# Kernel optimization log

Measured on AMD Instinct MI355X. Metric: run time of the kernel, lower is better.

Reference implementation:

```python
import jax, jax.numpy as jnp
import numpy as np

L, D, H, DH, I, S, B, MAXP, NFEAT = 4, 512, 4, 128, 128, 256, 128, 256, 6


def layer_norm(x, g, b):
    mu = jnp.mean(x, -1, keepdims=True)
    var = jnp.mean((x - mu) ** 2, -1, keepdims=True)
    return (x - mu) * jax.lax.rsqrt(var + 1e-12) * g + b


def setup_inputs() -> dict:
    key = jax.random.key(0)
    ks = iter(jax.random.split(key, 16))
    p = lambda shape: jax.random.normal(next(ks), shape, jnp.float32) * 0.02
    return dict(
        input_ids=jax.random.randint(next(ks), (B, S, NFEAT), 0, 64, jnp.int32),
        attn_mask=jnp.ones((B, S), jnp.float32),
        in_W=p((NFEAT, D)), in_b=jnp.zeros((D,), jnp.float32),
        tok_emb=p((D,)),  # token_type_embeddings row 0 (all-zero token type ids)
        emb_ln_g=jnp.ones((D,), jnp.float32), emb_ln_b=jnp.zeros((D,), jnp.float32),
        dist_emb=p((2 * MAXP - 1, DH)),
        Wq=p((L, D, D)), bq=jnp.zeros((L, D), jnp.float32),
        Wk=p((L, D, D)), bk=jnp.zeros((L, D), jnp.float32),
        Wv=p((L, D, D)), bv=jnp.zeros((L, D), jnp.float32),
        Wo=p((L, D, D)), bo=jnp.zeros((L, D), jnp.float32),
        ln1_g=jnp.ones((L, D), jnp.float32), ln1_b=jnp.zeros((L, D), jnp.float32),
        Wi=p((L, D, I)), bi=jnp.zeros((L, I), jnp.float32),
        Wo2=p((L, I, D)), bo2=jnp.zeros((L, D), jnp.float32),
        ln2_g=jnp.ones((L, D), jnp.float32), ln2_b=jnp.zeros((L, D), jnp.float32),
    )


def reference(input_ids, attn_mask, in_W, in_b, tok_emb, emb_ln_g, emb_ln_b,
              dist_emb, Wq, bq, Wk, bk, Wv, bv, Wo, bo, ln1_g, ln1_b,
              Wi, bi, Wo2, bo2, ln2_g, ln2_b):
    # in_linear on raw float features, then BertEmbeddings (no absolute pos emb
    # since position_embedding_type='relative_key_query'), token_type 0 + LN.
    x = input_ids.astype(jnp.float32) @ in_W + in_b          # [B,S,D]
    x = layer_norm(x + tok_emb, emb_ln_g, emb_ln_b)
    # relative position embeddings: distance l-r, table index shifted by MAXP-1
    pos = jnp.arange(S)
    pe = dist_emb[pos[:, None] - pos[None, :] + MAXP - 1]    # [S,S,DH]
    bias = (1.0 - attn_mask)[:, None, None, :] * jnp.float32(-1e9)
    scale = jnp.float32(1.0 / np.sqrt(DH))
    for l in range(L):
        q = (x @ Wq[l] + bq[l]).reshape(B, S, H, DH).transpose(0, 2, 1, 3)
        k = (x @ Wk[l] + bk[l]).reshape(B, S, H, DH).transpose(0, 2, 1, 3)
        v = (x @ Wv[l] + bv[l]).reshape(B, S, H, DH).transpose(0, 2, 1, 3)
        scores = jnp.einsum('bhld,bhrd->bhlr', q, k)
        scores = scores + jnp.einsum('bhld,lrd->bhlr', q, pe)  # relative_key_query: query term
        scores = scores + jnp.einsum('bhrd,lrd->bhlr', k, pe)  # key term
        probs = jax.nn.softmax(scores * scale + bias, axis=-1)
        ctx = jnp.einsum('bhlr,bhrd->bhld', probs, v)
        ctx = ctx.transpose(0, 2, 1, 3).reshape(B, S, D)
        x = layer_norm(x + ctx @ Wo[l] + bo[l], ln1_g[l], ln1_b[l])
        h = jax.nn.gelu(x @ Wi[l] + bi[l], approximate=False)
        x = layer_norm(x + h @ Wo2[l] + bo2[l], ln2_g[l], ln2_b[l])
    return x  # last_hidden_state [B,S,D]
```

## Files before the change

### kernel.cpp

```cpp
#include <hip/hip_runtime.h>

typedef unsigned short u16;
typedef __bf16 bf16x8 __attribute__((ext_vector_type(8)));
typedef float f32x4 __attribute__((ext_vector_type(4)));

__device__ __forceinline__ float b2f(u16 u) { return __uint_as_float(((unsigned)u) << 16); }
__device__ __forceinline__ u16 f2b(float f) {
  unsigned i = __float_as_uint(f);
  return (u16)((i + 0x7FFFu + ((i >> 16) & 1u)) >> 16);
}
__device__ __forceinline__ float sane(float x, float lim) {
  float y = fminf(fmaxf(x, -lim), lim);
  return (y != y) ? 0.0f : y;
}
__device__ __forceinline__ float wred(float x) {
#pragma unroll
  for (int m = 1; m < 64; m <<= 1) x += __shfl_xor(x, m, 64);
  return x;
}

__device__ __forceinline__ void bar_lgkm() {
  asm volatile("s_waitcnt lgkmcnt(0)" ::: "memory");
  __builtin_amdgcn_s_barrier();
  asm volatile("" ::: "memory");
}

__global__ void detect_dtype(const unsigned* __restrict__ g_ones, int* __restrict__ flag) {
  *flag = (g_ones[0] == 0x3F800000u) ? 1 : 0;
}

#define NSEG 23
struct CvtArgs {
  const void* src[NSEG];
  int start[NSEG + 1];
};
__global__ __launch_bounds__(256) void cvt_all(CvtArgs a, u16* __restrict__ dst,
                                               const int* __restrict__ flag) {
  const int i = blockIdx.x * 256 + threadIdx.x;
  if (i >= a.start[NSEG]) return;
  int k = 0;
#pragma unroll
  for (int s = 1; s < NSEG; ++s) k += (i >= a.start[s]) ? 1 : 0;
  const int j = i - a.start[k];
  u16 v;
  if (*flag) v = f2b(((const float*)a.src[k])[j]);
  else       v = ((const u16*)a.src[k])[j];
  dst[i] = v;
}

__global__ __launch_bounds__(256) void transpose_bf16(const u16* __restrict__ src,
                                                      u16* __restrict__ dst, int R, int C) {
  __shared__ u16 tile[32][33];
  const long zo = (long)blockIdx.z * R * C;
  src += zo; dst += zo;
  const int tx = threadIdx.x & 31, ty = threadIdx.x >> 5;
  const int c0 = blockIdx.x * 32, r0 = blockIdx.y * 32;
#pragma unroll
  for (int i = 0; i < 32; i += 8) tile[ty + i][tx] = src[(r0 + ty + i) * C + c0 + tx];
  __syncthreads();
#pragma unroll
  for (int i = 0; i < 32; i += 8) dst[(c0 + ty + i) * R + r0 + tx] = tile[tx][ty + i];
}

__global__ __launch_bounds__(256) void embed_ln(const int* __restrict__ ids,
    const u16* __restrict__ inW, const u16* __restrict__ inB, const u16* __restrict__ tokE,
    const u16* __restrict__ g, const u16* __restrict__ bb, u16* __restrict__ xb) {
  const int wave = threadIdx.x >> 6, lane = threadIdx.x & 63;
  const int n = blockIdx.x * 4 + wave;
  float idv[6];
#pragma unroll
  for (int f = 0; f < 6; ++f) idv[f] = (float)ids[n * 6 + f];
  float v[8]; float s = 0.f;
#pragma unroll
  for (int j = 0; j < 8; ++j) {
    const int d = j * 64 + lane;
    float a = b2f(inB[d]) + b2f(tokE[d]);
#pragma unroll
    for (int f = 0; f < 6; ++f) a += idv[f] * b2f(inW[f * 512 + d]);
    v[j] = a; s += a;
  }
  s = wred(s);
  const float mu = s * (1.f / 512.f);
  float q = 0.f;
#pragma unroll
  for (int j = 0; j < 8; ++j) { float t = v[j] - mu; q += t * t; }
  q = wred(q);
  const float rstd = rsqrtf(q * (1.f / 512.f) + 1e-12f);
#pragma unroll
  for (int j = 0; j < 8; ++j) {
    const int d = j * 64 + lane;
    xb[n * 512 + d] = f2b(sane((v[j] - mu) * rstd * b2f(g[d]) + b2f(bb[d]), 6e4f));
  }
}

__global__ __launch_bounds__(256) void add_ln(const u16* __restrict__ xin,
    const u16* __restrict__ add, const u16* __restrict__ g, const u16* __restrict__ bb,
    void* __restrict__ outp, const int* __restrict__ flag, int isfinal) {
  const int wave = threadIdx.x >> 6, lane = threadIdx.x & 63;
  const int n = blockIdx.x * 4 + wave;
  const int base = n * 512 + lane * 8;
  uint4 xa = *(const uint4*)&xin[base];
  uint4 aa = *(const uint4*)&add[base];
  const unsigned* xw = (const unsigned*)&xa;
  const unsigned* aw = (const unsigned*)&aa;
  float v[8]; float s = 0.f;
#pragma unroll
  for (int w = 0; w < 4; ++w) {
    float x0 = b2f((u16)(xw[w] & 0xffff)) + b2f((u16)(aw[w] & 0xffff));
    float x1 = b2f((u16)(xw[w] >> 16)) + b2f((u16)(aw[w] >> 16));
    v[w * 2] = x0; v[w * 2 + 1] = x1; s += x0 + x1;
  }
  s = wred(s);
  const float mu = s * (1.f / 512.f);
  float qs = 0.f;
#pragma unroll
  for (int j = 0; j < 8; ++j) { float t = v[j] - mu; qs += t * t; }
  qs = wred(qs);
  const float rstd = rsqrtf(qs * (1.f / 512.f) + 1e-12f);
  uint4 ga = *(const uint4*)&g[lane * 8];
  uint4 ba = *(const uint4*)&bb[lane * 8];
  const unsigned* gw = (const unsigned*)&ga;
  const unsigned* bw = (const unsigned*)&ba;
  float y[8];
#pragma unroll
  for (int w = 0; w < 4; ++w) {
    y[w * 2]     = sane((v[w * 2] - mu) * rstd * b2f((u16)(gw[w] & 0xffff)) + b2f((u16)(bw[w] & 0xffff)), 6e4f);
    y[w * 2 + 1] = sane((v[w * 2 + 1] - mu) * rstd * b2f((u16)(gw[w] >> 16)) + b2f((u16)(bw[w] >> 16)), 6e4f);
  }
  if (isfinal && *flag) {
    float* of = (float*)outp;
    float4 o0, o1;
    o0.x = y[0]; o0.y = y[1]; o0.z = y[2]; o0.w = y[3];
    o1.x = y[4]; o1.y = y[5]; o1.z = y[6]; o1.w = y[7];
    *(float4*)&of[base] = o0;
    *(float4*)&of[base + 4] = o1;
  } else {
    uint4 o;
    unsigned* ow = (unsigned*)&o;
#pragma unroll
    for (int w = 0; w < 4; ++w)
      ow[w] = (unsigned)f2b(y[w * 2]) | ((unsigned)f2b(y[w * 2 + 1]) << 16);
    *(uint4*)&((u16*)outp)[base] = o;
  }
}

enum { EPI_ROW, EPI_GELU, EPI_QKH, EPI_VT, EPI_B2, EPI_B3 };

typedef __attribute__((address_space(1))) const char gld_g;
typedef __attribute__((address_space(3))) char gld_l;

template <int EPI>
__global__ __launch_bounds__(256)
void gemm_bt(const u16* __restrict__ A, const u16* __restrict__ BT,
             const u16* __restrict__ bias, u16* __restrict__ out, int K, int ldo) {
  __shared__ alignas(16) u16 sT[2 * 128 * 64];
  u16* sA = sT;
  u16* sB = sT + 128 * 64;
  const int tid = threadIdx.x;
  const int wave = tid >> 6, lane = tid & 63;
  const int quad = lane >> 4, li = lane & 15;
  const int m0 = blockIdx.x * 128, n0 = blockIdx.y * 128;
  const u16* Ab = A + (size_t)m0 * K;
  const u16* Bb = BT + (size_t)n0 * K;
  const int wm = wave >> 1, wn = wave & 1;
  const int lrow = lane >> 3;
  const int lchk = (lane & 7) ^ lrow;
  f32x4 acc[4][4] = {};
  for (int kt = 0; kt < K; kt += 64) {
    if (kt) __syncthreads();
#pragma unroll
    for (int i = 0; i < 4; ++i) {
      const int r = wave * 32 + i * 8 + lrow;
      __builtin_amdgcn_global_load_lds(
          (gld_g*)(Ab + (size_t)r * K + kt + lchk * 8),
          (gld_l*)&sA[(wave * 32 + i * 8) * 64], 16, 0, 0);
      __builtin_amdgcn_global_load_lds(
          (gld_g*)(Bb + (size_t)r * K + kt + lchk * 8),
          (gld_l*)&sB[(wave * 32 + i * 8) * 64], 16, 0, 0);
    }
    asm volatile("s_waitcnt vmcnt(0)" ::: "memory");
    __syncthreads();
#pragma unroll
    for (int h = 0; h < 2; ++h) {
      bf16x8 aF[4], bF[4];
#pragma unroll
      for (int mt = 0; mt < 4; ++mt) {
        const int r = wm * 64 + mt * 16 + li;
        aF[mt] = *(const bf16x8*)&sA[r * 64 + ((h * 32 + quad * 8) ^ ((r & 7) << 3))];
      }
#pragma unroll
      for (int nt = 0; nt < 4; ++nt) {
        const int r = wn * 64 + nt * 16 + li;
        bF[nt] = *(const bf16x8*)&sB[r * 64 + ((h * 32 + quad * 8) ^ ((r & 7) << 3))];
      }
#pragma unroll
      for (int mt = 0; mt < 4; ++mt)
#pragma unroll
        for (int nt = 0; nt < 4; ++nt)
          acc[mt][nt] = __builtin_amdgcn_mfma_f32_16x16x32_bf16(aF[mt], bF[nt], acc[mt][nt], 0, 0, 0);
    }
  }
  if constexpr (EPI == EPI_VT) {
    __syncthreads();
#pragma unroll
    for (int mt = 0; mt < 4; ++mt)
#pragma unroll
      for (int nt = 0; nt < 4; ++nt)
#pragma unroll
        for (int r = 0; r < 4; ++r) {
          const int ml = wm * 64 + mt * 16 + quad * 4 + r;
          const int nl = wn * 64 + nt * 16 + li;
          float v = sane(acc[mt][nt][r] + b2f(bias[n0 + nl]), 6e4f);
          sT[nl * 128 + (ml ^ ((nl & 7) << 3))] = f2b(v);
        }
    __syncthreads();
    const int bht = (m0 >> 8) * 4 + (n0 >> 7);
    const int s0 = m0 & 255;
    const int dh = tid >> 1, half = tid & 1;
    u16* orow = out + ((size_t)bht * 128 + dh) * 256 + s0 + half * 64;
#pragma unroll
    for (int i = 0; i < 8; ++i) {
      const int idx = dh * 128 + ((half * 64 + i * 8) ^ ((dh & 7) << 3));
      *(uint4*)&orow[i * 8] = *(const uint4*)&sT[idx];
    }
  } else if constexpr (EPI == EPI_B2 || EPI == EPI_B3) {
#pragma unroll
    for (int mt = 0; mt < 4; ++mt) {
#pragma unroll
      for (int nt = 0; nt < 4; ++nt) {
#pragma unroll
        for (int r = 0; r < 4; ++r) {
          const int m = m0 + wm * 64 + mt * 16 + quad * 4 + r;
          const int n = n0 + wn * 64 + nt * 16 + li;
          float v = sane(acc[mt][nt][r], 1e4f);
          const int ll = m & 255;
          if constexpr (EPI == EPI_B2) {
            const int rr2 = ll - n + 255;
            if ((unsigned)rr2 < 256u) out[(size_t)m * 256 + rr2] = f2b(v);
          } else {
            const int lo = n + ll - 255;
            if ((unsigned)lo < 256u) out[(size_t)m * 256 + lo] = f2b(v);
          }
        }
      }
    }
  } else {
#pragma unroll
    for (int mt = 0; mt < 4; ++mt) {
#pragma unroll
      for (int nt = 0; nt < 4; ++nt) {
#pragma unroll
        for (int r = 0; r < 4; ++r) {
          const int m = m0 + wm * 64 + mt * 16 + quad * 4 + r;
          const int n = n0 + wn * 64 + nt * 16 + li;
          float v = sane(acc[mt][nt][r] + b2f(bias[n]), 6e4f);
          if constexpr (EPI == EPI_GELU) v = 0.5f * v * (1.0f + erff(v * 0.70710678118654752f));
          if constexpr (EPI == EPI_ROW || EPI == EPI_GELU) {
            out[m * ldo + n] = f2b(v);
          } else {
            out[(((m >> 8) * 4 + (n >> 7)) * 256 + (m & 255)) * 128 + (n & 127)] = f2b(v);
          }
        }
      }
    }
  }
}

__global__ __launch_bounds__(256, 3)
void attn_kernel(const u16* __restrict__ qb, const u16* __restrict__ kb,
                 const u16* __restrict__ vtb, const u16* __restrict__ b2g,
                 const u16* __restrict__ b3g, const u16* __restrict__ mask,
                 u16* __restrict__ ctx) {
  __shared__ alignas(16) u16 sKV[9216];
  __shared__ alignas(16) u16 sP[16896];
  char* sPb = (char*)sP;
  const int tid = threadIdx.x;
  const int wave = tid >> 6, lane = tid & 63, quad = lane >> 4, li = lane & 15;
  const int lt = blockIdx.x;
  const int bh = blockIdx.y;
  const int b = bh >> 2, h = bh & 3;
  const int l0 = lt * 64;
  const u16* Qg = qb + (size_t)bh * 256 * 128;
  const u16* Kg = kb + (size_t)bh * 256 * 128;
  const u16* Vg = vtb + (size_t)bh * 128 * 256;
  const u16* B2g = b2g + (size_t)bh * 256 * 256;
  const u16* B3g = b3g + (size_t)bh * 256 * 256;
  const float scale = 0.08838834764831845f;

  const int krow = tid >> 2, kq4 = tid & 3;
  uint4 kreg[2][4];
#pragma unroll
  for (int i = 0; i < 4; ++i)
    kreg[0][i] = *(const uint4*)&Kg[krow * 128 + kq4 * 8 + i * 32];
  uint4 breg[2][2];
#pragma unroll
  for (int h2 = 0; h2 < 2; ++h2)
    breg[0][h2] = *(const uint4*)&B3g[(size_t)krow * 256 + l0 + kq4 * 16 + h2 * 8];

  bf16x8 aQ[4];
#pragma unroll
  for (int kt = 0; kt < 4; ++kt)
    aQ[kt] = *(const bf16x8*)&Qg[(l0 + wave * 16 + li) * 128 + kt * 32 + quad * 8];

  f32x4 sc[16] = {};
#pragma unroll
  for (int c = 0; c < 4; ++c) {
    if (c > 0) bar_lgkm();
#pragma unroll
    for (int i = 0; i < 4; ++i)
      *(uint4*)&sKV[krow * 136 + kq4 * 8 + i * 32] = kreg[c & 1][i];
#pragma unroll
    for (int h2 = 0; h2 < 2; ++h2)
      *(uint4*)&sPb[c * 8192 + ((krow * 128 + kq4 * 32 + h2 * 16) ^ ((krow & 7) << 4))] =
          breg[c & 1][h2];
    u16 b2v[16];
#pragma unroll
    for (int t2 = 0; t2 < 4; ++t2)
#pragma unroll
      for (int rr = 0; rr < 4; ++rr)
        b2v[t2 * 4 + rr] =
            B2g[(size_t)(l0 + wave * 16 + quad * 4 + rr) * 256 + c * 64 + t2 * 16 + li];
    if (c < 3) {
#pragma unroll
      for (int i = 0; i < 4; ++i)
        kreg[(c + 1) & 1][i] =
            *(const uint4*)&Kg[((c + 1) * 64 + krow) * 128 + kq4 * 8 + i * 32];
#pragma unroll
      for (int h2 = 0; h2 < 2; ++h2)
        breg[(c + 1) & 1][h2] =
            *(const uint4*)&B3g[(size_t)((c + 1) * 64 + krow) * 256 + l0 + kq4 * 16 + h2 * 8];
    }
    bar_lgkm();
    __builtin_amdgcn_s_setprio(1);
#pragma unroll
    for (int kt = 0; kt < 4; ++kt) {
#pragma unroll
      for (int nt = 0; nt < 4; ++nt) {
        bf16x8 bK = *(const bf16x8*)&sKV[(nt * 16 + li) * 136 + kt * 32 + quad * 8];
        sc[c * 4 + nt] = __builtin_amdgcn_mfma_f32_16x16x32_bf16(aQ[kt], bK, sc[c * 4 + nt], 0, 0, 0);
      }
    }
    __builtin_amdgcn_s_setprio(0);
#pragma unroll
    for (int t2 = 0; t2 < 4; ++t2)
#pragma unroll
      for (int rr = 0; rr < 4; ++rr) {
        const int myl = wave * 16 + quad * 4 + rr;
        const int R = t2 * 16 + li;
        float v3 = b2f(*(const u16*)&sPb[c * 8192 + ((R * 128 + myl * 2) ^ ((R & 7) << 4))]);
        float v2 = b2f(b2v[t2 * 4 + rr]);
        sc[c * 4 + t2][rr] += v2 + v3;
      }
  }

  const int vrow = tid >> 1, vhalf = tid & 1;
  uint4 vreg[2][4];
#pragma unroll
  for (int i = 0; i < 4; ++i)
    vreg[0][i] = *(const uint4*)&Vg[vrow * 256 + vhalf * 32 + i * 8];

  float mbv[16];
#pragma unroll
  for (int t = 0; t < 16; ++t)
    mbv[t] = (1.0f - b2f(mask[b * 256 + t * 16 + li])) * -1e9f;

#pragma unroll
  for (int t = 0; t < 16; ++t)
#pragma unroll
    for (int r = 0; r < 4; ++r) sc[t][r] = sane(sc[t][r] * scale + mbv[t], 2e9f);
#pragma unroll
  for (int r = 0; r < 4; ++r) {
    float mx = -3.0e38f;
#pragma unroll
    for (int t = 0; t < 16; ++t) mx = fmaxf(mx, sc[t][r]);
#pragma unroll
    for (int m = 1; m < 16; m <<= 1) mx = fmaxf(mx, __shfl_xor(mx, m, 64));
    float s = 0.f;
#pragma unroll
    for (int t = 0; t < 16; ++t) { float e = __expf(sc[t][r] - mx); sc[t][r] = e; s += e; }
#pragma unroll
    for (int m = 1; m < 16; m <<= 1) s += __shfl_xor(s, m, 64);
    const float inv = 1.f / s;
#pragma unroll
    for (int t = 0; t < 16; ++t) sc[t][r] *= inv;
  }

  bar_lgkm();
#pragma unroll
  for (int t = 0; t < 16; ++t)
#pragma unroll
    for (int r = 0; r < 4; ++r)
      sP[(wave * 16 + quad * 4 + r) * 264 + t * 16 + li] = f2b(sc[t][r]);

  f32x4 ct[8] = {};
#pragma unroll
  for (int c = 0; c < 4; ++c) {
    if (c > 0) bar_lgkm();
#pragma unroll
    for (int i = 0; i < 4; ++i)
      *(uint4*)&sKV[vrow * 72 + vhalf * 32 + i * 8] = vreg[c & 1][i];
    if (c < 3) {
#pragma unroll
      for (int i = 0; i < 4; ++i)
        vreg[(c + 1) & 1][i] =
            *(const uint4*)&Vg[vrow * 256 + (c + 1) * 64 + vhalf * 32 + i * 8];
    }
    bar_lgkm();
    __builtin_amdgcn_s_setprio(1);
#pragma unroll
    for (int ks = 0; ks < 2; ++ks) {
      bf16x8 aF = *(const bf16x8*)&sP[(wave * 16 + li) * 264 + c * 64 + ks * 32 + quad * 8];
#pragma unroll
      for (int nt = 0; nt < 8; ++nt) {
        bf16x8 bV = *(const bf16x8*)&sKV[(nt * 16 + li) * 72 + ks * 32 + quad * 8];
        ct[nt] = __builtin_amdgcn_mfma_f32_16x16x32_bf16(aF, bV, ct[nt], 0, 0, 0);
      }
    }
    __builtin_amdgcn_s_setprio(0);
  }

  bar_lgkm();
#pragma unroll
  for (int nt = 0; nt < 8; ++nt)
#pragma unroll
    for (int r = 0; r < 4; ++r)
      sP[(wave * 16 + quad * 4 + r) * 136 + nt * 16 + li] = f2b(sane(ct[nt][r], 1e4f));
  bar_lgkm();
  {
    const int row = tid >> 2, seg = tid & 3;
    u16* orow = ctx + ((size_t)(b * 256 + l0 + row)) * 512 + h * 128 + seg * 32;
    const u16* srow = &sP[row * 136 + seg * 32];
#pragma unroll
    for (int i = 0; i < 4; ++i)
      *(uint4*)&orow[i * 8] = *(const uint4*)&srow[i * 8];
  }
}

extern "C" void kernel_launch(void* const* d_in, const int* in_sizes, int n_in,
                              void* d_out, int out_size, void* d_ws, size_t ws_size,
                              hipStream_t stream) {
  (void)in_sizes; (void)n_in; (void)out_size; (void)ws_size;
  const int* ids = (const int*)d_in[0];

  static const int ns[NSEG] = {
      32768, 3072, 512, 512, 512, 512, 65408,
      1048576, 2048, 1048576, 2048, 1048576, 2048, 1048576, 2048,
      2048, 2048, 262144, 512, 262144, 2048, 2048, 2048
  };
  CvtArgs ca;
  int st[NSEG + 1];
  st[0] = 0;
  for (int k = 0; k < NSEG; ++k) { ca.src[k] = d_in[k + 1]; st[k + 1] = st[k] + ns[k]; }
  for (int k = 0; k <= NSEG; ++k) ca.start[k] = st[k];
  const int total = st[NSEG];

  char* W = (char*)d_ws;
  size_t off = 0;
  auto alloc = [&](size_t bytes) { void* p = W + off; off += (bytes + 255) & ~(size_t)255; return p; };
  u16* canon = (u16*)alloc((size_t)total * 2);
  int* flag  = (int*)alloc(256);
  const size_t ND = (size_t)32768 * 512;
  u16* xb   = (u16*)alloc(ND * 2);
  u16* qbf  = (u16*)alloc(ND * 2);
  u16* kbf  = (u16*)alloc(ND * 2);
  u16* vtb  = (u16*)alloc(ND * 2);
  u16* b2b  = (u16*)alloc((size_t)32768 * 256 * 2);
  u16* b3b  = (u16*)alloc((size_t)32768 * 256 * 2);
  u16* wqT  = (u16*)alloc((size_t)4 * 512 * 512 * 2);
  u16* wkT  = (u16*)alloc((size_t)4 * 512 * 512 * 2);
  u16* wvT  = (u16*)alloc((size_t)4 * 512 * 512 * 2);
  u16* woT  = (u16*)alloc((size_t)4 * 512 * 512 * 2);
  u16* wiT  = (u16*)alloc((size_t)4 * 512 * 128 * 2);
  u16* wo2T = (u16*)alloc((size_t)4 * 128 * 512 * 2);
  u16* ctxb = (u16*)d_out;

  const u16* mask = canon + st[0];
  const u16* inW  = canon + st[1];
  const u16* inB  = canon + st[2];
  const u16* tokE = canon + st[3];
  const u16* eg   = canon + st[4];
  const u16* ebb  = canon + st[5];
  const u16* de   = canon + st[6];
  const u16* Wq   = canon + st[7];
  const u16* bq   = canon + st[8];
  const u16* Wk   = canon + st[9];
  const u16* bk   = canon + st[10];
  const u16* Wv   = canon + st[11];
  const u16* bv   = canon + st[12];
  const u16* Wo   = canon + st[13];
  const u16* bo   = canon + st[14];
  const u16* l1g  = canon + st[15];
  const u16* l1b  = canon + st[16];
  const u16* Wi   = canon + st[17];
  const u16* bi   = canon + st[18];
  const u16* Wo2  = canon + st[19];
  const u16* bo2  = canon + st[20];
  const u16* l2g  = canon + st[21];
  const u16* l2b  = canon + st[22];

  dim3 B256(256);
  detect_dtype<<<1, 1, 0, stream>>>((const unsigned*)d_in[5], flag);
  cvt_all<<<(total + 255) / 256, B256, 0, stream>>>(ca, canon, flag);
  transpose_bf16<<<dim3(16, 16, 4), B256, 0, stream>>>(Wq, wqT, 512, 512);
  transpose_bf16<<<dim3(16, 16, 4), B256, 0, stream>>>(Wk, wkT, 512, 512);
  transpose_bf16<<<dim3(16, 16, 4), B256, 0, stream>>>(Wv, wvT, 512, 512);
  transpose_bf16<<<dim3(16, 16, 4), B256, 0, stream>>>(Wo, woT, 512, 512);
  transpose_bf16<<<dim3(4, 16, 4), B256, 0, stream>>>(Wi, wiT, 512, 128);
  transpose_bf16<<<dim3(16, 4, 4), B256, 0, stream>>>(Wo2, wo2T, 128, 512);
  embed_ln<<<8192, B256, 0, stream>>>(ids, inW, inB, tokE, eg, ebb, xb);

  for (int l = 0; l < 4; ++l) {
    gemm_bt<EPI_QKH><<<dim3(256, 4), B256, 0, stream>>>(xb, wqT + l * 512 * 512, bq + l * 512, qbf, 512, 0);
    gemm_bt<EPI_QKH><<<dim3(256, 4), B256, 0, stream>>>(xb, wkT + l * 512 * 512, bk + l * 512, kbf, 512, 0);
    gemm_bt<EPI_B2><<<dim3(256, 4), B256, 0, stream>>>(qbf, de, bq, b2b, 128, 0);
    gemm_bt<EPI_B3><<<dim3(256, 4), B256, 0, stream>>>(kbf, de, bk, b3b, 128, 0);
    gemm_bt<EPI_VT><<<dim3(256, 4), B256, 0, stream>>>(xb, wvT + l * 512 * 512, bv + l * 512, vtb, 512, 0);
    attn_kernel<<<dim3(4, 512), B256, 0, stream>>>(qbf, kbf, vtb, b2b, b3b, mask, ctxb);
    gemm_bt<EPI_ROW><<<dim3(256, 4), B256, 0, stream>>>(ctxb, woT + l * 512 * 512, bo + l * 512, qbf, 512, 512);
    add_ln<<<8192, B256, 0, stream>>>(xb, qbf, l1g + l * 512, l1b + l * 512, xb, flag, 0);
    gemm_bt<EPI_GELU><<<dim3(256, 1), B256, 0, stream>>>(xb, wiT + l * 512 * 128, bi + l * 128, kbf, 512, 128);
    gemm_bt<EPI_ROW><<<dim3(256, 4), B256, 0, stream>>>(kbf, wo2T + l * 128 * 512, bo2 + l * 512, vtb, 128, 512);
    add_ln<<<8192, B256, 0, stream>>>(xb, vtb, l2g + l * 512, l2b + l * 512,
                                      (l == 3) ? d_out : (void*)xb, flag, (l == 3) ? 1 : 0);
  }
}
```

Baseline: 1.320 ms.

## Fuse QKV projection, band-limit relative-position GEMMs, chunk attention by head quarter

Merges the Q, K and V projection GEMMs into a single launch over a concatenated transposed weight, with per-column-block epilogues. Replaces the two full relative-position GEMMs with one band kernel that only computes the three 128-wide distance tiles each row block actually needs, dropping a quarter of that work. Interleaves the band GEMM and attention over four quarters of the batch-heads so the bias intermediates being consumed are smaller and more likely to stay cached. This adds launches per layer and adds branching in the fused epilogue.

```diff
diff --git a/kernel.cpp b/kernel.cpp
--- a/kernel.cpp
+++ b/kernel.cpp
@@ -49,10 +49,11 @@
 }
 
 __global__ __launch_bounds__(256) void transpose_bf16(const u16* __restrict__ src,
-                                                      u16* __restrict__ dst, int R, int C) {
+                                                      u16* __restrict__ dst, int R, int C,
+                                                      long dstride) {
   __shared__ u16 tile[32][33];
-  const long zo = (long)blockIdx.z * R * C;
-  src += zo; dst += zo;
+  src += (long)blockIdx.z * R * C;
+  dst += (long)blockIdx.z * dstride;
   const int tx = threadIdx.x & 31, ty = threadIdx.x >> 5;
   const int c0 = blockIdx.x * 32, r0 = blockIdx.y * 32;
 #pragma unroll
@@ -144,10 +145,55 @@
   }
 }
 
-enum { EPI_ROW, EPI_GELU, EPI_QKH, EPI_VT, EPI_B2, EPI_B3 };
+enum { EPI_ROW, EPI_GELU };
 
 typedef __attribute__((address_space(1))) const char gld_g;
 typedef __attribute__((address_space(3))) char gld_l;
+
+#define GEMM_PROLOG                                             \
+  const int tid = threadIdx.x;                                  \
+  const int wave = tid >> 6, lane = tid & 63;                   \
+  const int quad = lane >> 4, li = lane & 15;                   \
+  const int wm = wave >> 1, wn = wave & 1;                      \
+  const int lrow = lane >> 3;                                   \
+  const int lchk = (lane & 7) ^ lrow;
+
+#define GEMM_KLOOP(KK)                                                              \
+  f32x4 acc[4][4] = {};                                                             \
+  for (int kt = 0; kt < (KK); kt += 64) {                                           \
+    if (kt) __syncthreads();                                                        \
+    _Pragma("unroll")                                                               \
+    for (int i = 0; i < 4; ++i) {                                                   \
+      const int r = wave * 32 + i * 8 + lrow;                                       \
+      __builtin_amdgcn_global_load_lds(                                             \
+          (gld_g*)(Ab + (size_t)r * (KK) + kt + lchk * 8),                          \
+          (gld_l*)&sA[(wave * 32 + i * 8) * 64], 16, 0, 0);                         \
+      __builtin_amdgcn_global_load_lds(                                             \
+          (gld_g*)(Bb + (size_t)r * (KK) + kt + lchk * 8),                          \
+          (gld_l*)&sB[(wave * 32 + i * 8) * 64], 16, 0, 0);                         \
+    }                                                                               \
+    asm volatile("s_waitcnt vmcnt(0)" ::: "memory");                                \
+    __syncthreads();                                                                \
+    _Pragma("unroll")                                                               \
+    for (int h = 0; h < 2; ++h) {                                                   \
+      bf16x8 aF[4], bF[4];                                                          \
+      _Pragma("unroll")                                                             \
+      for (int mt = 0; mt < 4; ++mt) {                                              \
+        const int r = wm * 64 + mt * 16 + li;                                       \
+        aF[mt] = *(const bf16x8*)&sA[r * 64 + ((h * 32 + quad * 8) ^ ((r & 7) << 3))]; \
+      }                                                                             \
+      _Pragma("unroll")                                                             \
+      for (int nt = 0; nt < 4; ++nt) {                                              \
+        const int r = wn * 64 + nt * 16 + li;                                       \
+        bF[nt] = *(const bf16x8*)&sB[r * 64 + ((h * 32 + quad * 8) ^ ((r & 7) << 3))]; \
+      }                                                                             \
+      _Pragma("unroll")                                                             \
+      for (int mt = 0; mt < 4; ++mt)                                                \
+        _Pragma("unroll")                                                           \
+        for (int nt = 0; nt < 4; ++nt)                                              \
+          acc[mt][nt] = __builtin_amdgcn_mfma_f32_16x16x32_bf16(aF[mt], bF[nt], acc[mt][nt], 0, 0, 0); \
+    }                                                                               \
+  }
 
 template <int EPI>
 __global__ __launch_bounds__(256)
@@ -156,51 +202,42 @@
   __shared__ alignas(16) u16 sT[2 * 128 * 64];
   u16* sA = sT;
   u16* sB = sT + 128 * 64;
-  const int tid = threadIdx.x;
-  const int wave = tid >> 6, lane = tid & 63;
-  const int quad = lane >> 4, li = lane & 15;
+  GEMM_PROLOG
   const int m0 = blockIdx.x * 128, n0 = blockIdx.y * 128;
   const u16* Ab = A + (size_t)m0 * K;
   const u16* Bb = BT + (size_t)n0 * K;
-  const int wm = wave >> 1, wn = wave & 1;
-  const int lrow = lane >> 3;
-  const int lchk = (lane & 7) ^ lrow;
-  f32x4 acc[4][4] = {};
-  for (int kt = 0; kt < K; kt += 64) {
-    if (kt) __syncthreads();
-#pragma unroll
-    for (int i = 0; i < 4; ++i) {
-      const int r = wave * 32 + i * 8 + lrow;
-      __builtin_amdgcn_global_load_lds(
-          (gld_g*)(Ab + (size_t)r * K + kt + lchk * 8),
-          (gld_l*)&sA[(wave * 32 + i * 8) * 64], 16, 0, 0);
-      __builtin_amdgcn_global_load_lds(
-          (gld_g*)(Bb + (size_t)r * K + kt + lchk * 8),
-          (gld_l*)&sB[(wave * 32 + i * 8) * 64], 16, 0, 0);
-    }
-    asm volatile("s_waitcnt vmcnt(0)" ::: "memory");
-    __syncthreads();
-#pragma unroll
-    for (int h = 0; h < 2; ++h) {
-      bf16x8 aF[4], bF[4];
-#pragma unroll
-      for (int mt = 0; mt < 4; ++mt) {
-        const int r = wm * 64 + mt * 16 + li;
-        aF[mt] = *(const bf16x8*)&sA[r * 64 + ((h * 32 + quad * 8) ^ ((r & 7) << 3))];
+  GEMM_KLOOP(K)
+#pragma unroll
+  for (int mt = 0; mt < 4; ++mt) {
+#pragma unroll
+    for (int nt = 0; nt < 4; ++nt) {
+#pragma unroll
+      for (int r = 0; r < 4; ++r) {
+        const int m = m0 + wm * 64 + mt * 16 + quad * 4 + r;
+        const int n = n0 + wn * 64 + nt * 16 + li;
+        float v = sane(acc[mt][nt][r] + b2f(bias[n]), 6e4f);
+        if constexpr (EPI == EPI_GELU) v = 0.5f * v * (1.0f + erff(v * 0.70710678118654752f));
+        out[m * ldo + n] = f2b(v);
       }
-#pragma unroll
-      for (int nt = 0; nt < 4; ++nt) {
-        const int r = wn * 64 + nt * 16 + li;
-        bF[nt] = *(const bf16x8*)&sB[r * 64 + ((h * 32 + quad * 8) ^ ((r & 7) << 3))];
-      }
-#pragma unroll
-      for (int mt = 0; mt < 4; ++mt)
-#pragma unroll
-        for (int nt = 0; nt < 4; ++nt)
-          acc[mt][nt] = __builtin_amdgcn_mfma_f32_16x16x32_bf16(aF[mt], bF[nt], acc[mt][nt], 0, 0, 0);
-    }
-  }
-  if constexpr (EPI == EPI_VT) {
+    }
+  }
+}
+
+__global__ __launch_bounds__(256)
+void gemm_qkv(const u16* __restrict__ A, const u16* __restrict__ BT,
+              const u16* __restrict__ bq, const u16* __restrict__ bk,
+              const u16* __restrict__ bv, u16* __restrict__ qo,
+              u16* __restrict__ ko, u16* __restrict__ vo) {
+  __shared__ alignas(16) u16 sT[2 * 128 * 64];
+  u16* sA = sT;
+  u16* sB = sT + 128 * 64;
+  GEMM_PROLOG
+  const int m0 = blockIdx.x * 128, n0 = blockIdx.y * 128;
+  const u16* Ab = A + (size_t)m0 * 512;
+  const u16* Bb = BT + (size_t)n0 * 512;
+  GEMM_KLOOP(512)
+  const int which = n0 >> 9, nb = n0 & 511;
+  if (which == 2) {
     __syncthreads();
 #pragma unroll
     for (int mt = 0; mt < 4; ++mt)
@@ -210,20 +247,22 @@
         for (int r = 0; r < 4; ++r) {
           const int ml = wm * 64 + mt * 16 + quad * 4 + r;
           const int nl = wn * 64 + nt * 16 + li;
-          float v = sane(acc[mt][nt][r] + b2f(bias[n0 + nl]), 6e4f);
+          float v = sane(acc[mt][nt][r] + b2f(bv[nb + nl]), 6e4f);
           sT[nl * 128 + (ml ^ ((nl & 7) << 3))] = f2b(v);
         }
     __syncthreads();
-    const int bht = (m0 >> 8) * 4 + (n0 >> 7);
+    const int bht = (m0 >> 8) * 4 + (nb >> 7);
     const int s0 = m0 & 255;
     const int dh = tid >> 1, half = tid & 1;
-    u16* orow = out + ((size_t)bht * 128 + dh) * 256 + s0 + half * 64;
+    u16* orow = vo + ((size_t)bht * 128 + dh) * 256 + s0 + half * 64;
 #pragma unroll
     for (int i = 0; i < 8; ++i) {
       const int idx = dh * 128 + ((half * 64 + i * 8) ^ ((dh & 7) << 3));
       *(uint4*)&orow[i * 8] = *(const uint4*)&sT[idx];
     }
-  } else if constexpr (EPI == EPI_B2 || EPI == EPI_B3) {
+  } else {
+    u16* o = which ? ko : qo;
+    const u16* bi = which ? bk : bq;
 #pragma unroll
     for (int mt = 0; mt < 4; ++mt) {
 #pragma unroll
@@ -231,35 +270,46 @@
 #pragma unroll
         for (int r = 0; r < 4; ++r) {
           const int m = m0 + wm * 64 + mt * 16 + quad * 4 + r;
-          const int n = n0 + wn * 64 + nt * 16 + li;
-          float v = sane(acc[mt][nt][r], 1e4f);
-          const int ll = m & 255;
-          if constexpr (EPI == EPI_B2) {
-            const int rr2 = ll - n + 255;
-            if ((unsigned)rr2 < 256u) out[(size_t)m * 256 + rr2] = f2b(v);
-          } else {
-            const int lo = n + ll - 255;
-            if ((unsigned)lo < 256u) out[(size_t)m * 256 + lo] = f2b(v);
-          }
+          const int n = nb + wn * 64 + nt * 16 + li;
+          float v = sane(acc[mt][nt][r] + b2f(bi[n]), 6e4f);
+          o[(((m >> 8) * 4 + (n >> 7)) * 256 + (m & 255)) * 128 + (n & 127)] = f2b(v);
         }
       }
     }
-  } else {
-#pragma unroll
-    for (int mt = 0; mt < 4; ++mt) {
-#pragma unroll
-      for (int nt = 0; nt < 4; ++nt) {
-#pragma unroll
-        for (int r = 0; r < 4; ++r) {
-          const int m = m0 + wm * 64 + mt * 16 + quad * 4 + r;
-          const int n = n0 + wn * 64 + nt * 16 + li;
-          float v = sane(acc[mt][nt][r] + b2f(bias[n]), 6e4f);
-          if constexpr (EPI == EPI_GELU) v = 0.5f * v * (1.0f + erff(v * 0.70710678118654752f));
-          if constexpr (EPI == EPI_ROW || EPI == EPI_GELU) {
-            out[m * ldo + n] = f2b(v);
-          } else {
-            out[(((m >> 8) * 4 + (n >> 7)) * 256 + (m & 255)) * 128 + (n & 127)] = f2b(v);
-          }
+  }
+}
+
+__global__ __launch_bounds__(256)
+void gemm_band(const u16* __restrict__ qq, const u16* __restrict__ kq,
+               const u16* __restrict__ de, u16* __restrict__ b2o,
+               u16* __restrict__ b3o) {
+  __shared__ alignas(16) u16 sT[2 * 128 * 64];
+  u16* sA = sT;
+  u16* sB = sT + 128 * 64;
+  GEMM_PROLOG
+  const int half = blockIdx.x >> 8;
+  const int mi = (blockIdx.x & 255) * 128;
+  const int s0 = mi & 255;
+  const int p0 = (half ? 128 - s0 : s0) + blockIdx.y * 128;
+  const u16* Ab = (half ? kq : qq) + (size_t)mi * 128;
+  const u16* Bb = de + (size_t)p0 * 128;
+  GEMM_KLOOP(128)
+#pragma unroll
+  for (int mt = 0; mt < 4; ++mt) {
+#pragma unroll
+    for (int nt = 0; nt < 4; ++nt) {
+#pragma unroll
+      for (int r = 0; r < 4; ++r) {
+        const int m = mi + wm * 64 + mt * 16 + quad * 4 + r;
+        const int n = p0 + wn * 64 + nt * 16 + li;
+        float v = sane(acc[mt][nt][r], 1e4f);
+        const int ll = m & 255;
+        if (!half) {
+          const int rr2 = ll - n + 255;
+          if ((unsigned)rr2 < 256u) b2o[(size_t)m * 256 + rr2] = f2b(v);
+        } else {
+          const int lo = n + ll - 255;
+          if ((unsigned)lo < 256u) b3o[(size_t)m * 256 + lo] = f2b(v);
         }
       }
     }
@@ -270,21 +320,22 @@
 void attn_kernel(const u16* __restrict__ qb, const u16* __restrict__ kb,
                  const u16* __restrict__ vtb, const u16* __restrict__ b2g,
                  const u16* __restrict__ b3g, const u16* __restrict__ mask,
-                 u16* __restrict__ ctx) {
+                 u16* __restrict__ ctx, int bh0) {
   __shared__ alignas(16) u16 sKV[9216];
   __shared__ alignas(16) u16 sP[16896];
   char* sPb = (char*)sP;
   const int tid = threadIdx.x;
   const int wave = tid >> 6, lane = tid & 63, quad = lane >> 4, li = lane & 15;
   const int lt = blockIdx.x;
-  const int bh = blockIdx.y;
+  const int bhl = blockIdx.y;
+  const int bh = bhl + bh0;
   const int b = bh >> 2, h = bh & 3;
   const int l0 = lt * 64;
   const u16* Qg = qb + (size_t)bh * 256 * 128;
   const u16* Kg = kb + (size_t)bh * 256 * 128;
   const u16* Vg = vtb + (size_t)bh * 128 * 256;
-  const u16* B2g = b2g + (size_t)bh * 256 * 256;
-  const u16* B3g = b3g + (size_t)bh * 256 * 256;
+  const u16* B2g = b2g + (size_t)bhl * 256 * 256;
+  const u16* B3g = b3g + (size_t)bhl * 256 * 256;
   const float scale = 0.08838834764831845f;
 
   const int krow = tid >> 2, kq4 = tid & 3;
@@ -460,19 +511,17 @@
   u16* canon = (u16*)alloc((size_t)total * 2);
   int* flag  = (int*)alloc(256);
   const size_t ND = (size_t)32768 * 512;
-  u16* xb   = (u16*)alloc(ND * 2);
-  u16* qbf  = (u16*)alloc(ND * 2);
-  u16* kbf  = (u16*)alloc(ND * 2);
-  u16* vtb  = (u16*)alloc(ND * 2);
-  u16* b2b  = (u16*)alloc((size_t)32768 * 256 * 2);
-  u16* b3b  = (u16*)alloc((size_t)32768 * 256 * 2);
-  u16* wqT  = (u16*)alloc((size_t)4 * 512 * 512 * 2);
-  u16* wkT  = (u16*)alloc((size_t)4 * 512 * 512 * 2);
-  u16* wvT  = (u16*)alloc((size_t)4 * 512 * 512 * 2);
-  u16* woT  = (u16*)alloc((size_t)4 * 512 * 512 * 2);
-  u16* wiT  = (u16*)alloc((size_t)4 * 512 * 128 * 2);
-  u16* wo2T = (u16*)alloc((size_t)4 * 128 * 512 * 2);
-  u16* ctxb = (u16*)d_out;
+  u16* xb    = (u16*)alloc(ND * 2);
+  u16* qbf   = (u16*)alloc(ND * 2);
+  u16* kbf   = (u16*)alloc(ND * 2);
+  u16* vtb   = (u16*)alloc(ND * 2);
+  u16* b2b   = (u16*)alloc((size_t)32768 * 256 * 2);
+  u16* b3b   = (u16*)alloc((size_t)32768 * 256 * 2);
+  u16* wqkvT = (u16*)alloc((size_t)4 * 1536 * 512 * 2);
+  u16* woT   = (u16*)alloc((size_t)4 * 512 * 512 * 2);
+  u16* wiT   = (u16*)alloc((size_t)4 * 512 * 128 * 2);
+  u16* wo2T  = (u16*)alloc((size_t)4 * 128 * 512 * 2);
+  u16* ctxb  = (u16*)d_out;
 
   const u16* mask = canon + st[0];
   const u16* inW  = canon + st[1];
@@ -501,21 +550,24 @@
   dim3 B256(256);
   detect_dtype<<<1, 1, 0, stream>>>((const unsigned*)d_in[5], flag);
   cvt_all<<<(total + 255) / 256, B256, 0, stream>>>(ca, canon, flag);
-  transpose_bf16<<<dim3(16, 16, 4), B256, 0, stream>>>(Wq, wqT, 512, 512);
-  transpose_bf16<<<dim3(16, 16, 4), B256, 0, stream>>>(Wk, wkT, 512, 512);
-  transpose_bf16<<<dim3(16, 16, 4), B256, 0, stream>>>(Wv, wvT, 512, 512);
-  transpose_bf16<<<dim3(16, 16, 4), B256, 0, stream>>>(Wo, woT, 512, 512);
-  transpose_bf16<<<dim3(4, 16, 4), B256, 0, stream>>>(Wi, wiT, 512, 128);
-  transpose_bf16<<<dim3(16, 4, 4), B256, 0, stream>>>(Wo2, wo2T, 128, 512);
+  transpose_bf16<<<dim3(16, 16, 4), B256, 0, stream>>>(Wq, wqkvT, 512, 512, 1536L * 512);
+  transpose_bf16<<<dim3(16, 16, 4), B256, 0, stream>>>(Wk, wqkvT + 512 * 512, 512, 512, 1536L * 512);
+  transpose_bf16<<<dim3(16, 16, 4), B256, 0, stream>>>(Wv, wqkvT + 1024 * 512, 512, 512, 1536L * 512);
+  transpose_bf16<<<dim3(16, 16, 4), B256, 0, stream>>>(Wo, woT, 512, 512, 512L * 512);
+  transpose_bf16<<<dim3(4, 16, 4), B256, 0, stream>>>(Wi, wiT, 512, 128, 512L * 128);
+  transpose_bf16<<<dim3(16, 4, 4), B256, 0, stream>>>(Wo2, wo2T, 128, 512, 128L * 512);
   embed_ln<<<8192, B256, 0, stream>>>(ids, inW, inB, tokE, eg, ebb, xb);
 
   for (int l = 0; l < 4; ++l) {
-    gemm_bt<EPI_QKH><<<dim3(256, 4), B256, 0, stream>>>(xb, wqT + l * 512 * 512, bq + l * 512, qbf, 512, 0);
-    gemm_bt<EPI_QKH><<<dim3(256, 4), B256, 0, stream>>>(xb, wkT + l * 512 * 512, bk + l * 512, kbf, 512, 0);
-    gemm_bt<EPI_B2><<<dim3(256, 4), B256, 0, stream>>>(qbf, de, bq, b2b, 128, 0);
-    gemm_bt<EPI_B3><<<dim3(256, 4), B256, 0, stream>>>(kbf, de, bk, b3b, 128, 0);
-    gemm_bt<EPI_VT><<<dim3(256, 4), B256, 0, stream>>>(xb, wvT + l * 512 * 512, bv + l * 512, vtb, 512, 0);
-    attn_kernel<<<dim3(4, 512), B256, 0, stream>>>(qbf, kbf, vtb, b2b, b3b, mask, ctxb);
+    gemm_qkv<<<dim3(256, 12), B256, 0, stream>>>(xb, wqkvT + (size_t)l * 1536 * 512,
+                                                 bq + l * 512, bk + l * 512, bv + l * 512,
+                                                 qbf, kbf, vtb);
+    for (int q = 0; q < 4; ++q) {
+      const size_t qoff = (size_t)q * 128 * 256 * 128;
+      gemm_band<<<dim3(512, 3), B256, 0, stream>>>(qbf + qoff, kbf + qoff, de, b2b, b3b);
+      attn_kernel<<<dim3(4, 128), B256, 0, stream>>>(qbf, kbf, vtb, b2b, b3b, mask, ctxb,
+                                                     q * 128);
+    }
     gemm_bt<EPI_ROW><<<dim3(256, 4), B256, 0, stream>>>(ctxb, woT + l * 512 * 512, bo + l * 512, qbf, 512, 512);
     add_ln<<<8192, B256, 0, stream>>>(xb, qbf, l1g + l * 512, l1b + l * 512, xb, flag, 0);
     gemm_bt<EPI_GELU><<<dim3(256, 1), B256, 0, stream>>>(xb, wiT + l * 512 * 128, bi + l * 128, kbf, 512, 128);
```

New measurement: 1.602 ms. 1.21x slower.
